# Optimization experiments

Hardware: AMD Instinct MI355X
Metric: run time of the kernel (lower is better)

The kernel has to match this reference:

```python
import jax, jax.numpy as jnp
import numpy as np

N_SPATIAL = 3          # config.N_spatial_dim
N_POL = 2              # config.N_polarizations
DT = 0.1               # config.simulation_config.dt
EPS = 1e-8

N_NODES = 100000
N_EDGES = 1600000
IN_DIM = 16
MSG_DIM = 128


def setup_inputs() -> dict:
    key = jax.random.key(0)
    ks = jax.random.split(key, 6)
    x = jax.random.normal(ks[0], (N_NODES, IN_DIM), dtype=jnp.float32)
    edge_index = jax.random.randint(ks[1], (2, N_EDGES), 0, N_NODES, dtype=jnp.int64)
    W_msg = jax.random.normal(ks[2], (IN_DIM, MSG_DIM), dtype=jnp.float32) * (1.0 / np.sqrt(IN_DIM))
    b_msg = jax.random.normal(ks[3], (MSG_DIM,), dtype=jnp.float32) * 0.01
    W_out = jax.random.normal(ks[4], (MSG_DIM, IN_DIM), dtype=jnp.float32) * (1.0 / np.sqrt(MSG_DIM))
    b_out = jax.random.normal(ks[5], (IN_DIM,), dtype=jnp.float32) * 0.01
    return {"x": x, "edge_index": edge_index, "W_msg": W_msg, "b_msg": b_msg,
            "W_out": W_out, "b_out": b_out, "steps": 4}


def _step(x, src, dst, W_msg, b_msg, W_out, b_out):
    # message_conv: per-node transform, gather at source, scatter-sum at destination
    h = x @ W_msg + b_msg                                   # [N, MSG_DIM]
    messages = jax.ops.segment_sum(h[src], dst, num_segments=N_NODES)  # [N, MSG_DIM]
    # message_to_output: Linear(MSG_DIM -> IN_DIM)
    output = messages @ W_out + b_out                       # [N, IN_DIM]
    # update: residual Euler step + L2-normalize polarization slice
    x = x + output * DT
    start, end = N_SPATIAL, N_SPATIAL + 2 * N_POL
    pol = x[:, start:end]
    norm = jnp.sqrt(jnp.sum(pol * pol, axis=1, keepdims=True))
    pol = pol / jnp.maximum(norm, EPS)                      # F.normalize(p=2, eps=1e-8)
    return jnp.concatenate((x[:, :start], pol, x[:, end:]), axis=1)


def reference(x, edge_index, W_msg, b_msg, W_out, b_out, steps):
    src, dst = edge_index[0], edge_index[1]
    for _ in range(steps):
        x = _step(x, src, dst, W_msg, b_msg, W_out, b_out)
    return x
```

## Files before the change

kernel.cpp:

```cpp
#include <hip/hip_runtime.h>

#define NN 100000
#define NE 1600000
#define IN_DIM 16
#define MSG_DIM 128
#define DT_C 0.1f
#define EPS_C 1e-8f
#define BKT 128
#define NB ((NN + BKT - 1) / BKT)
#define EPB 6400
#define NBB (NE / EPB)
#define EPT (EPB / 256)
#define CAPB 4096
#define CAP 2560

__device__ __forceinline__ float blo(unsigned c) { return __uint_as_float(c << 16); }
__device__ __forceinline__ float bhi(unsigned c) { return __uint_as_float(c & 0xFFFF0000u); }
__device__ __forceinline__ unsigned short f2b(float f) {
    unsigned int i = __float_as_uint(f);
    unsigned int b = i + 0x7FFFu + ((i >> 16) & 1u);
    return (unsigned short)(b >> 16);
}

__global__ void compute_wc_kernel(const float* __restrict__ W_msg,
                                  const float* __restrict__ b_msg,
                                  const float* __restrict__ W_out,
                                  float* __restrict__ Wc,
                                  float* __restrict__ bc) {
    int t = threadIdx.x;
    int i = t >> 4, j = t & 15;
    float s = 0.f;
    for (int k = 0; k < MSG_DIM; ++k)
        s += W_msg[i * MSG_DIM + k] * W_out[k * IN_DIM + j];
    Wc[t] = s;
    if (t < IN_DIM) {
        float sb = 0.f;
        for (int k = 0; k < MSG_DIM; ++k)
            sb += b_msg[k] * W_out[k * IN_DIM + t];
        bc[t] = sb;
    }
}

__global__ void cvt_kernel(const float* __restrict__ x, unsigned* __restrict__ xb) {
    int i = blockIdx.x * blockDim.x + threadIdx.x;
    if (i * 2 >= NN * IN_DIM) return;
    float2 v = ((const float2*)x)[i];
    xb[i] = (unsigned)f2b(v.x) | ((unsigned)f2b(v.y) << 16);
}

__global__ void init782_kernel(int* __restrict__ gcur) {
    int t = blockIdx.x * blockDim.x + threadIdx.x;
    if (t < NB) gcur[t] = t * CAPB;
}

__global__ __launch_bounds__(256) void bucketA_kernel(const int* __restrict__ src,
                                                      const int* __restrict__ dst,
                                                      int* __restrict__ gcur,
                                                      unsigned* __restrict__ bucket) {
    __shared__ int lcnt[NB];
    __shared__ int lbase[NB];
    int t = threadIdx.x;
    for (int j = t; j < NB; j += 256) lcnt[j] = 0;
    __syncthreads();

    int d[EPT], s[EPT];
    int base = blockIdx.x * EPB + t;
    #pragma unroll
    for (int it = 0; it < EPT; ++it) {
        d[it] = dst[base + it * 256];
        s[it] = src[base + it * 256];
    }
    #pragma unroll
    for (int it = 0; it < EPT; ++it) atomicAdd(&lcnt[d[it] >> 7], 1);
    __syncthreads();
    for (int j = t; j < NB; j += 256) {
        int c = lcnt[j];
        lbase[j] = c ? atomicAdd(&gcur[j], c) : 0;
        lcnt[j] = 0;
    }
    __syncthreads();
    #pragma unroll
    for (int it = 0; it < EPT; ++it) {
        int b = d[it] >> 7;
        int slot = atomicAdd(&lcnt[b], 1);
        bucket[lbase[b] + slot] = ((unsigned)(d[it] & 127) << 17) | (unsigned)s[it];
    }
}

__global__ __launch_bounds__(1024) void scan782_kernel(const int* __restrict__ gcur,
                                                       int* __restrict__ gbase,
                                                       int* __restrict__ offs) {
    __shared__ int sh[1024];
    int t = threadIdx.x;
    int v = (t < NB) ? (gcur[t] - t * CAPB) : 0;
    sh[t] = v;
    __syncthreads();
    #pragma unroll
    for (int off = 1; off < 1024; off <<= 1) {
        int u = (t >= off) ? sh[t - off] : 0;
        __syncthreads();
        sh[t] += u;
        __syncthreads();
    }
    if (t < NB) gbase[t] = sh[t] - v;
    if (t == 0) { gbase[NB] = NE; offs[NN] = NE; }
}

__global__ __launch_bounds__(256) void bucket2csr_kernel(const unsigned* __restrict__ bucket,
                                                         const int* __restrict__ gcur,
                                                         const int* __restrict__ gbase,
                                                         int* __restrict__ offs,
                                                         int* __restrict__ csr) {
    __shared__ int lcnt[BKT];
    __shared__ int ls[BKT];
    __shared__ int lcur[BKT];
    __shared__ int lcsr[CAP];
    int b = blockIdx.x;
    int t = threadIdx.x;
    int p0 = b * CAPB;
    int len = gcur[b] - p0;
    int g0 = gbase[b];
    if (t < BKT) lcnt[t] = 0;
    __syncthreads();
    for (int i = t; i < len; i += 256)
        atomicAdd(&lcnt[bucket[p0 + i] >> 17], 1);
    __syncthreads();
    if (t < BKT) ls[t] = lcnt[t];
    __syncthreads();
    #pragma unroll
    for (int off = 1; off < BKT; off <<= 1) {
        int u = (t < BKT && t >= off) ? ls[t - off] : 0;
        __syncthreads();
        if (t < BKT) ls[t] += u;
        __syncthreads();
    }
    if (t < BKT) {
        int ex = ls[t] - lcnt[t];
        lcur[t] = ex;
        int n = b * BKT + t;
        if (n < NN) offs[n] = g0 + ex;
    }
    __syncthreads();
    if (len <= CAP) {
        for (int i = t; i < len; i += 256) {
            unsigned pk = bucket[p0 + i];
            int pos = atomicAdd(&lcur[pk >> 17], 1);
            lcsr[pos] = (int)(pk & 0x1FFFFu);
        }
        __syncthreads();
        for (int i = t; i < len; i += 256) csr[g0 + i] = lcsr[i];
    } else {
        for (int i = t; i < len; i += 256) {
            unsigned pk = bucket[p0 + i];
            int pos = atomicAdd(&lcur[pk >> 17], 1);
            csr[g0 + pos] = (int)(pk & 0x1FFFFu);
        }
    }
}

__global__ __launch_bounds__(256) void step_kernel(const float2* __restrict__ x2in,
                                                   const uint4* __restrict__ xbin,
                                                   const int* __restrict__ offs,
                                                   const int* __restrict__ csr,
                                                   const float* __restrict__ Wc,
                                                   const float* __restrict__ bc,
                                                   const float* __restrict__ b_out,
                                                   float2* __restrict__ x2out,
                                                   unsigned* __restrict__ xbout) {
    __shared__ float sWc[256];
    __shared__ float sbc[16];
    __shared__ float sb[16];
    int t = threadIdx.x;
    sWc[t] = Wc[t];
    if (t < 16) { sbc[t] = bc[t]; sb[t] = b_out[t]; }
    __syncthreads();

    int tid = blockIdx.x * 256 + t;
    int n = tid >> 3;
    int l = t & 7;
    int p = l >> 1;
    int hf = l & 1;
    if (n >= NN) return;

    int o0 = offs[n];
    int o1 = offs[n + 1];

    float acc[8];
    #pragma unroll
    for (int j = 0; j < 8; ++j) acc[j] = 0.f;

    for (int e = o0 + p; e < o1; e += 4) {
        int s = csr[e];
        uint4 v = xbin[s * 2 + hf];
        acc[0] += blo(v.x); acc[1] += bhi(v.x);
        acc[2] += blo(v.y); acc[3] += bhi(v.y);
        acc[4] += blo(v.z); acc[5] += bhi(v.z);
        acc[6] += blo(v.w); acc[7] += bhi(v.w);
    }

    #pragma unroll
    for (int j = 0; j < 8; ++j) {
        acc[j] += __shfl_xor(acc[j], 2);
        acc[j] += __shfl_xor(acc[j], 4);
    }
    float a[16];
    #pragma unroll
    for (int j = 0; j < 8; ++j) {
        float oth = __shfl_xor(acc[j], 1);
        a[j]     = hf ? oth    : acc[j];
        a[8 + j] = hf ? acc[j] : oth;
    }

    float dg = (float)(o1 - o0);

    int c0 = 2 * l;
    float o0f = dg * sbc[c0] + sb[c0];
    float o1f = dg * sbc[c0 + 1] + sb[c0 + 1];
    #pragma unroll
    for (int k = 0; k < 16; ++k) {
        float ak = a[k];
        o0f = fmaf(ak, sWc[k * 16 + c0], o0f);
        o1f = fmaf(ak, sWc[k * 16 + c0 + 1], o1f);
    }

    float2 xv = x2in[(size_t)n * 8 + l];
    float xn0 = xv.x + DT_C * o0f;
    float xn1 = xv.y + DT_C * o1f;

    bool in0 = (c0 >= 3 && c0 <= 6);
    bool in1 = (c0 + 1 >= 3 && c0 + 1 <= 6);
    float ssp = (in0 ? xn0 * xn0 : 0.f) + (in1 ? xn1 * xn1 : 0.f);
    ssp += __shfl_xor(ssp, 1);
    ssp += __shfl_xor(ssp, 2);
    ssp += __shfl_xor(ssp, 4);
    float sc = 1.0f / fmaxf(sqrtf(ssp), EPS_C);
    if (in0) xn0 *= sc;
    if (in1) xn1 *= sc;

    x2out[(size_t)n * 8 + l] = make_float2(xn0, xn1);
    xbout[(size_t)n * 8 + l] = (unsigned)f2b(xn0) | ((unsigned)f2b(xn1) << 16);
}

extern "C" void kernel_launch(void* const* d_in, const int* in_sizes, int n_in,
                              void* d_out, int out_size, void* d_ws, size_t ws_size,
                              hipStream_t stream) {
    const float* x0    = (const float*)d_in[0];
    const int*   ei    = (const int*)d_in[1];
    const float* W_msg = (const float*)d_in[2];
    const float* b_msg = (const float*)d_in[3];
    const float* W_out = (const float*)d_in[4];
    const float* b_out = (const float*)d_in[5];

    float* X = (float*)d_out;

    float*          Y      = (float*)d_ws;
    unsigned*       xb0    = (unsigned*)(Y + (size_t)NN * IN_DIM);
    unsigned*       xb1    = xb0 + (size_t)NN * (IN_DIM / 2);
    unsigned*       bucket = xb1 + (size_t)NN * (IN_DIM / 2);
    int*            csr    = (int*)(bucket + (size_t)NB * CAPB);
    int*            offs   = csr + NE;
    int*            gbase  = offs + NN + 1;
    int*            gcur   = gbase + NB + 1;
    float*          Wc     = (float*)(gcur + NB);
    float*          bc     = Wc + 256;

    const int* src = ei;
    const int* dst = ei + NE;

    compute_wc_kernel<<<1, 256, 0, stream>>>(W_msg, b_msg, W_out, Wc, bc);
    cvt_kernel<<<(NN * IN_DIM / 2 + 255) / 256, 256, 0, stream>>>(x0, xb0);
    init782_kernel<<<(NB + 255) / 256, 256, 0, stream>>>(gcur);
    bucketA_kernel<<<NBB, 256, 0, stream>>>(src, dst, gcur, bucket);
    scan782_kernel<<<1, 1024, 0, stream>>>(gcur, gbase, offs);
    bucket2csr_kernel<<<NB, 256, 0, stream>>>(bucket, gcur, gbase, offs, csr);

    const int step_threads = NN * 8;
    const int step_blocks = (step_threads + 255) / 256;

    const float*    fin[4]  = { x0,  Y,   X,   Y  };
    float*          fout[4] = { Y,   X,   Y,   X  };
    const unsigned* bin[4]  = { xb0, xb1, xb0, xb1 };
    unsigned*       bout[4] = { xb1, xb0, xb1, xb0 };
    for (int s = 0; s < 4; ++s) {
        step_kernel<<<step_blocks, 256, 0, stream>>>(
            (const float2*)fin[s], (const uint4*)bin[s], offs, csr,
            Wc, bc, b_out, (float2*)fout[s], bout[s]);
    }
}
```

Measured before the change: 128.9 us.

## Unroll edge gather by two, fuse gcur init into convert, shrink bucketing tile

The per-node gather loop now handles two edges per iteration, so two independent index and row loads are in flight at once to hide gather latency. The gcur initialisation is folded into the bf16 conversion kernel, which removes one launch. Edges per bucketing block drop from 6400 to 2560, giving more blocks for parallelism at the cost of more global atomics and more per-block setup of the shared counters.

```diff
diff --git a/kernel.cpp b/kernel.cpp
--- a/kernel.cpp
+++ b/kernel.cpp
@@ -8,7 +8,7 @@
 #define EPS_C 1e-8f
 #define BKT 128
 #define NB ((NN + BKT - 1) / BKT)
-#define EPB 6400
+#define EPB 2560
 #define NBB (NE / EPB)
 #define EPT (EPB / 256)
 #define CAPB 4096
@@ -41,16 +41,13 @@
     }
 }
 
-__global__ void cvt_kernel(const float* __restrict__ x, unsigned* __restrict__ xb) {
+__global__ void cvt_kernel(const float* __restrict__ x, unsigned* __restrict__ xb,
+                           int* __restrict__ gcur) {
     int i = blockIdx.x * blockDim.x + threadIdx.x;
+    if (i < NB) gcur[i] = i * CAPB;
     if (i * 2 >= NN * IN_DIM) return;
     float2 v = ((const float2*)x)[i];
     xb[i] = (unsigned)f2b(v.x) | ((unsigned)f2b(v.y) << 16);
-}
-
-__global__ void init782_kernel(int* __restrict__ gcur) {
-    int t = blockIdx.x * blockDim.x + threadIdx.x;
-    if (t < NB) gcur[t] = t * CAPB;
 }
 
 __global__ __launch_bounds__(256) void bucketA_kernel(const int* __restrict__ src,
@@ -189,13 +186,29 @@
     #pragma unroll
     for (int j = 0; j < 8; ++j) acc[j] = 0.f;
 
-    for (int e = o0 + p; e < o1; e += 4) {
-        int s = csr[e];
-        uint4 v = xbin[s * 2 + hf];
-        acc[0] += blo(v.x); acc[1] += bhi(v.x);
-        acc[2] += blo(v.y); acc[3] += bhi(v.y);
-        acc[4] += blo(v.z); acc[5] += bhi(v.z);
-        acc[6] += blo(v.w); acc[7] += bhi(v.w);
+    int e = o0 + p;
+    while (e + 4 < o1) {
+        int s0 = csr[e];
+        int s1 = csr[e + 4];
+        uint4 v0 = xbin[s0 * 2 + hf];
+        uint4 v1 = xbin[s1 * 2 + hf];
+        acc[0] += blo(v0.x); acc[1] += bhi(v0.x);
+        acc[2] += blo(v0.y); acc[3] += bhi(v0.y);
+        acc[4] += blo(v0.z); acc[5] += bhi(v0.z);
+        acc[6] += blo(v0.w); acc[7] += bhi(v0.w);
+        acc[0] += blo(v1.x); acc[1] += bhi(v1.x);
+        acc[2] += blo(v1.y); acc[3] += bhi(v1.y);
+        acc[4] += blo(v1.z); acc[5] += bhi(v1.z);
+        acc[6] += blo(v1.w); acc[7] += bhi(v1.w);
+        e += 8;
+    }
+    if (e < o1) {
+        int s0 = csr[e];
+        uint4 v0 = xbin[s0 * 2 + hf];
+        acc[0] += blo(v0.x); acc[1] += bhi(v0.x);
+        acc[2] += blo(v0.y); acc[3] += bhi(v0.y);
+        acc[4] += blo(v0.z); acc[5] += bhi(v0.z);
+        acc[6] += blo(v0.w); acc[7] += bhi(v0.w);
     }
 
     #pragma unroll
@@ -268,8 +281,7 @@
     const int* dst = ei + NE;
 
     compute_wc_kernel<<<1, 256, 0, stream>>>(W_msg, b_msg, W_out, Wc, bc);
-    cvt_kernel<<<(NN * IN_DIM / 2 + 255) / 256, 256, 0, stream>>>(x0, xb0);
-    init782_kernel<<<(NB + 255) / 256, 256, 0, stream>>>(gcur);
+    cvt_kernel<<<(NN * IN_DIM / 2 + 255) / 256, 256, 0, stream>>>(x0, xb0, gcur);
     bucketA_kernel<<<NBB, 256, 0, stream>>>(src, dst, gcur, bucket);
     scan782_kernel<<<1, 1024, 0, stream>>>(gcur, gbase, offs);
     bucket2csr_kernel<<<NB, 256, 0, stream>>>(bucket, gcur, gbase, offs, csr);
```

New measurement: 129.7 us. Within noise of the previous version (+0.6%).
